# Kernel optimization log

Measured on AMD Instinct MI355X. Metric: run time of the kernel, lower is better.

## Reference

```python
import jax, jax.numpy as jnp
import numpy as np

V, D, T, B, H, L, FF = 32000, 1024, 1024, 2, 16, 2, 4096


def _ln(x, g, b, eps=1e-5):
    m = x.mean(-1, keepdims=True)
    v = ((x - m) ** 2).mean(-1, keepdims=True)
    return (x - m) * jax.lax.rsqrt(v + eps) * g + b


def setup_inputs() -> dict:
    key = jax.random.key(0)
    ks = jax.random.split(key, 16)
    s = 0.02  # init scale for stable softmax/logits
    return {
        "idx": jax.random.randint(ks[0], (B, T), 0, V),
        "targets": jax.random.randint(ks[1], (B, T), 0, V),
        "word_emb": jax.random.normal(ks[2], (V, D), jnp.float32) * s,
        "pos_emb": jax.random.normal(ks[3], (T, D), jnp.float32) * s,
        "ln1_g": jnp.ones((L, D), jnp.float32),
        "ln1_b": jnp.zeros((L, D), jnp.float32),
        "wq": jax.random.normal(ks[4], (L, D, D), jnp.float32) * s,
        "wk": jax.random.normal(ks[5], (L, D, D), jnp.float32) * s,
        "wv": jax.random.normal(ks[6], (L, D, D), jnp.float32) * s,
        "proj_w": jax.random.normal(ks[7], (L, D, D), jnp.float32) * s,
        "proj_b": jnp.zeros((L, D), jnp.float32),
        "ln2_g": jnp.ones((L, D), jnp.float32),
        "ln2_b": jnp.zeros((L, D), jnp.float32),
        "ff_w1": jax.random.normal(ks[8], (L, D, FF), jnp.float32) * s,
        "ff_b1": jnp.zeros((L, FF), jnp.float32),
        "ff_w2": jax.random.normal(ks[9], (L, FF, D), jnp.float32) * s,
        "ff_b2": jnp.zeros((L, D), jnp.float32),
        "lnf_g": jnp.ones((D,), jnp.float32),
        "lnf_b": jnp.zeros((D,), jnp.float32),
        "lm_w": jax.random.normal(ks[10], (D, V), jnp.float32) * s,
        "lm_b": jnp.zeros((V,), jnp.float32),
    }


def reference(word_emb, pos_emb, ln1_g, ln1_b, wq, wk, wv, proj_w, proj_b,
              ln2_g, ln2_b, ff_w1, ff_b1, ff_w2, ff_b2, lnf_g, lnf_b,
              lm_w, lm_b, idx, targets):
    b, t = idx.shape
    d = word_emb.shape[1]
    n_layer, n_head = wq.shape[0], H
    x = word_emb[idx] + pos_emb[:t]              # [B,T,D]
    causal = jnp.tril(jnp.ones((t, t), bool))
    maps = []
    for l in range(n_layer):
        h = _ln(x, ln1_g[l], ln1_b[l])
        q = (h @ wq[l]).reshape(b, t, n_head, -1)  # [B,T,H,hd]
        k = (h @ wk[l]).reshape(b, t, n_head, -1)
        v = (h @ wv[l]).reshape(b, t, n_head, -1)
        # NOTE: source scales by n_embd**-0.5 (full embedding dim), not head_size
        wei = jnp.einsum('bqhd,bkhd->bhqk', q, k) * (d ** -0.5)
        wei = jnp.where(causal, wei, -jnp.inf)
        wei = jax.nn.softmax(wei, axis=-1)        # [B,H,T,T]
        maps.append(wei)
        att = jnp.einsum('bhqk,bkhd->bqhd', wei, v).reshape(b, t, d)
        x = x + att @ proj_w[l] + proj_b[l]
        h2 = _ln(x, ln2_g[l], ln2_b[l])
        x = x + jax.nn.relu(h2 @ ff_w1[l] + ff_b1[l]) @ ff_w2[l] + ff_b2[l]
    x = _ln(x, lnf_g, lnf_b)
    logits = (x @ lm_w + lm_b).reshape(b * t, -1)  # [B*T, V]
    logp = jax.nn.log_softmax(logits, axis=-1)
    loss = -logp[jnp.arange(b * t), targets.reshape(-1)].mean()
    probs = jax.nn.log_softmax(x, axis=-1)         # source: LogSoftmax of final-LN x
    return (logits, loss, jnp.stack(maps), probs)
```

## Files before the change

### kernel.cpp

```cpp
#include <hip/hip_runtime.h>
#include <hip/hip_bf16.h>

#define VSZ 32000
#define DM  1024
#define TSEQ 1024
#define BB  2
#define HH  16
#define LL  2
#define FFD 4096
#define NTOK (BB*TSEQ)
#define QT  16

static constexpr size_t LOGITS_OFF = 0;
static constexpr size_t LOSS_OFF   = (size_t)NTOK * VSZ;
static constexpr size_t MAPS_OFF   = LOSS_OFF + 1;
static constexpr size_t PROBS_OFF  = MAPS_OFF + (size_t)LL*BB*HH*TSEQ*TSEQ;

typedef __attribute__((ext_vector_type(8))) short bf8;
typedef __attribute__((ext_vector_type(4))) float f32x4;
typedef __attribute__((ext_vector_type(4))) short short4v;

__device__ __forceinline__ short f2bf(float f) {
  union { float f; unsigned u; } v; v.f = f;
  unsigned r = v.u + 0x7FFFu + ((v.u >> 16) & 1u);
  return (short)(r >> 16);
}
__device__ __forceinline__ float bf2f(short s) {
  union { unsigned u; float f; } v; v.u = ((unsigned)(unsigned short)s) << 16;
  return v.f;
}

__device__ __forceinline__ void gload16(const void* g, void* l) {
  __builtin_amdgcn_global_load_lds(
      (const __attribute__((address_space(1))) void*)g,
      (__attribute__((address_space(3))) void*)l, 16, 0, 0);
}

__device__ __forceinline__ float block_sum256(float v, float* sh) {
#pragma unroll
  for (int off = 32; off; off >>= 1) v += __shfl_down(v, off);
  int wid = threadIdx.x >> 6, lane = threadIdx.x & 63;
  if (lane == 0) sh[wid] = v;
  __syncthreads();
  v = sh[0] + sh[1] + sh[2] + sh[3];
  __syncthreads();
  return v;
}
__device__ __forceinline__ float block_max256(float v, float* sh) {
#pragma unroll
  for (int off = 32; off; off >>= 1) v = fmaxf(v, __shfl_down(v, off));
  int wid = threadIdx.x >> 6, lane = threadIdx.x & 63;
  if (lane == 0) sh[wid] = v;
  __syncthreads();
  v = fmaxf(fmaxf(sh[0], sh[1]), fmaxf(sh[2], sh[3]));
  __syncthreads();
  return v;
}

static constexpr size_t PLW = (size_t)4 * DM * DM + (size_t)DM * FFD + (size_t)FFD * DM;
__global__ __launch_bounds__(256) void transpose_all(const float* __restrict__ wq,
    const float* __restrict__ wk, const float* __restrict__ wv,
    const float* __restrict__ proj_w, const float* __restrict__ ff_w1,
    const float* __restrict__ ff_w2, short* __restrict__ wt_base) {
  __shared__ float T[64][65];
  const int bid = blockIdx.x;
  const int l = bid / 3072, r = bid % 3072;
  short* qbase = wt_base + (size_t)l * PLW;
  const float* W; short* Wt; int K, N, tn, tk;
  if (r < 1024) {
    int s = r >> 8, rr = r & 255;
    W = (s == 0 ? wq : (s == 1 ? wk : (s == 2 ? wv : proj_w))) + (size_t)l * DM * DM;
    Wt = qbase + (size_t)s * DM * DM;
    K = DM; N = DM; tn = rr & 15; tk = rr >> 4;
  } else if (r < 2048) {
    int rr = r - 1024;
    W = ff_w1 + (size_t)l * DM * FFD; Wt = qbase + (size_t)4 * DM * DM;
    K = DM; N = FFD; tn = rr & 63; tk = rr >> 6;
  } else {
    int rr = r - 2048;
    W = ff_w2 + (size_t)l * FFD * DM; Wt = qbase + (size_t)4 * DM * DM + (size_t)DM * FFD;
    K = FFD; N = DM; tn = rr & 15; tk = rr >> 4;
  }
  const int n0 = tn * 64, k0 = tk * 64;
  const int tid = threadIdx.x;
  const int lr = tid >> 4, lc4 = (tid & 15) * 4;
#pragma unroll
  for (int p = 0; p < 4; ++p) {
    int k = lr + p * 16;
    float4 w = *(const float4*)&W[(size_t)(k0 + k) * N + n0 + lc4];
    T[k][lc4] = w.x; T[k][lc4+1] = w.y; T[k][lc4+2] = w.z; T[k][lc4+3] = w.w;
  }
  __syncthreads();
#pragma unroll
  for (int p = 0; p < 4; ++p) {
    int n = lr + p * 16;
    short4v s;
    s.x = f2bf(T[lc4  ][n]);
    s.y = f2bf(T[lc4+1][n]);
    s.z = f2bf(T[lc4+2][n]);
    s.w = f2bf(T[lc4+3][n]);
    *(short4v*)&Wt[(size_t)(n0 + n) * K + k0 + lc4] = s;
  }
}

__global__ __launch_bounds__(256) void transpose_cvt(const float* __restrict__ W,
    short* __restrict__ Wt, int K, int N) {
  __shared__ float T[64][65];
  const int n0 = blockIdx.x * 64, k0 = blockIdx.y * 64;
  const int tid = threadIdx.x;
  const int lr = tid >> 4, lc4 = (tid & 15) * 4;
#pragma unroll
  for (int p = 0; p < 4; ++p) {
    int k = lr + p * 16;
    float4 w = *(const float4*)&W[(size_t)(k0 + k) * N + n0 + lc4];
    T[k][lc4] = w.x; T[k][lc4+1] = w.y; T[k][lc4+2] = w.z; T[k][lc4+3] = w.w;
  }
  __syncthreads();
#pragma unroll
  for (int p = 0; p < 4; ++p) {
    int n = lr + p * 16;
    short4v s;
    s.x = f2bf(T[lc4  ][n]);
    s.y = f2bf(T[lc4+1][n]);
    s.z = f2bf(T[lc4+2][n]);
    s.w = f2bf(T[lc4+3][n]);
    *(short4v*)&Wt[(size_t)(n0 + n) * K + k0 + lc4] = s;
  }
}

__global__ __launch_bounds__(256) void embed_kernel(const int* __restrict__ idx,
    const float* __restrict__ we, const float* __restrict__ pe, float* __restrict__ x) {
  int i = blockIdx.x * 256 + threadIdx.x;
  int n = i >> 10;
  int d = i & 1023;
  int t = n & (TSEQ - 1);
  x[i] = we[(size_t)idx[n] * DM + d] + pe[(size_t)t * DM + d];
}

template<int ALSO_F32>
__global__ __launch_bounds__(256) void ln_bf(const float* __restrict__ in,
    const float* __restrict__ g, const float* __restrict__ b,
    short* __restrict__ outb, float* __restrict__ outf) {
  __shared__ float sh[4];
  int row = blockIdx.x, tid = threadIdx.x;
  const float* xr = in + (size_t)row * DM;
  float4 v = *(const float4*)&xr[tid * 4];
  float s  = v.x + v.y + v.z + v.w;
  float s2 = v.x*v.x + v.y*v.y + v.z*v.z + v.w*v.w;
  s  = block_sum256(s, sh);
  s2 = block_sum256(s2, sh);
  float mean = s * (1.0f / DM);
  float var  = s2 * (1.0f / DM) - mean * mean;
  float inv  = rsqrtf(var + 1e-5f);
  float4 gv = *(const float4*)&g[tid * 4];
  float4 bv = *(const float4*)&b[tid * 4];
  float4 o;
  o.x = (v.x - mean) * inv * gv.x + bv.x;
  o.y = (v.y - mean) * inv * gv.y + bv.y;
  o.z = (v.z - mean) * inv * gv.z + bv.z;
  o.w = (v.w - mean) * inv * gv.w + bv.w;
  short4v ob;
  ob.x = f2bf(o.x); ob.y = f2bf(o.y); ob.z = f2bf(o.z); ob.w = f2bf(o.w);
  *(short4v*)&outb[(size_t)row * DM + tid * 4] = ob;
  if (ALSO_F32)
    *(float4*)&outf[(size_t)row * DM + tid * 4] = o;
}

template<int BIAS, int RES, int RELU, int OUTBF>
__global__ __launch_bounds__(256) void gemm_bb(const short* __restrict__ A, int lda,
    const short* __restrict__ Bt, const float* __restrict__ bias,
    void* __restrict__ Cv, int M, int K, int Nn) {
  __shared__ short As[128 * 32];
  __shared__ short Bs[128 * 32];
  float* Cf = (float*)Cv;
  short* Cb = (short*)Cv;
  const int tid  = threadIdx.x;
  const int bm   = blockIdx.x * 128, bn = blockIdx.y * 128;
  const int lane = tid & 63, wid = tid >> 6;
  const int wr = wid >> 1, wc = wid & 1;
  const int lr = lane & 15, lg = lane >> 4;
  const int srow = lane >> 2;
  const int schunk = (lane & 3) * 8;

  f32x4 acc[4][4];
#pragma unroll
  for (int i = 0; i < 4; ++i)
#pragma unroll
    for (int j = 0; j < 4; ++j) acc[i][j] = (f32x4)0.f;

  for (int k0 = 0; k0 < K; k0 += 32) {
#pragma unroll
    for (int t = 0; t < 2; ++t) {
      const int issue = wid * 2 + t;
      const int row = issue * 16 + srow;
      gload16(&A[(size_t)(bm + row) * lda + k0 + schunk], &As[issue * 512]);
      gload16(&Bt[(size_t)(bn + row) * K  + k0 + schunk], &Bs[issue * 512]);
    }
    __syncthreads();
    bf8 af[4], bfv[4];
#pragma unroll
    for (int i = 0; i < 4; ++i)
      af[i] = *(const bf8*)&As[(wr * 64 + i * 16 + lr) * 32 + lg * 8];
#pragma unroll
    for (int j = 0; j < 4; ++j)
      bfv[j] = *(const bf8*)&Bs[(wc * 64 + j * 16 + lr) * 32 + lg * 8];
#pragma unroll
    for (int i = 0; i < 4; ++i)
#pragma unroll
      for (int j = 0; j < 4; ++j)
        acc[i][j] = __builtin_amdgcn_mfma_f32_16x16x32_bf16(af[i], bfv[j], acc[i][j], 0, 0, 0);
    __syncthreads();
  }
#pragma unroll
  for (int i = 0; i < 4; ++i) {
#pragma unroll
    for (int v = 0; v < 4; ++v) {
      int row = bm + wr * 64 + i * 16 + lg * 4 + v;
      size_t rowb = (size_t)row * Nn;
#pragma unroll
      for (int j = 0; j < 4; ++j) {
        int col = bn + wc * 64 + j * 16 + lr;
        float val = acc[i][j][v];
        if (BIAS) val += bias[col];
        if (RES)  val += Cf[rowb + col];
        if (RELU) val = fmaxf(val, 0.f);
        if (OUTBF) Cb[rowb + col] = f2bf(val);
        else       Cf[rowb + col] = val;
      }
    }
  }
}

template<int BIAS>
__global__ __launch_bounds__(256) void gemm_lm_cvt(const float* __restrict__ A,
    const float* __restrict__ Bw, const float* __restrict__ bias,
    float* __restrict__ C, int M, int K, int Nn) {
  __shared__ short As[128 * 40];
  __shared__ short Bs[128 * 40];
  const int tid  = threadIdx.x;
  const int bm   = blockIdx.x * 128, bn = blockIdx.y * 128;
  const int lane = tid & 63, wid = tid >> 6;
  const int wr = wid >> 1, wc = wid & 1;
  const int lr = lane & 15, lg = lane >> 4;
  const int sar = tid >> 3, sak = (tid & 7) * 4;
  const int sbn = tid & 127, sbk = (tid >> 7) * 16;
  f32x4 acc[4][4];
#pragma unroll
  for (int i = 0; i < 4; ++i)
#pragma unroll
    for (int j = 0; j < 4; ++j) acc[i][j] = (f32x4)0.f;
  for (int k0 = 0; k0 < K; k0 += 32) {
#pragma unroll
    for (int p = 0; p < 4; ++p) {
      int row = sar + p * 32;
      float4 a4 = *(const float4*)&A[(size_t)(bm + row) * K + k0 + sak];
      short4v s4;
      s4.x = f2bf(a4.x); s4.y = f2bf(a4.y); s4.z = f2bf(a4.z); s4.w = f2bf(a4.w);
      *(short4v*)&As[row * 40 + sak] = s4;
    }
    {
      short tmp[16];
#pragma unroll
      for (int e = 0; e < 16; ++e)
        tmp[e] = f2bf(Bw[(size_t)(k0 + sbk + e) * Nn + bn + sbn]);
      *(bf8*)&Bs[sbn * 40 + sbk    ] = *(bf8*)&tmp[0];
      *(bf8*)&Bs[sbn * 40 + sbk + 8] = *(bf8*)&tmp[8];
    }
    __syncthreads();
    bf8 af[4], bfv[4];
#pragma unroll
    for (int i = 0; i < 4; ++i)
      af[i] = *(const bf8*)&As[(wr * 64 + i * 16 + lr) * 40 + lg * 8];
#pragma unroll
    for (int j = 0; j < 4; ++j)
      bfv[j] = *(const bf8*)&Bs[(wc * 64 + j * 16 + lr) * 40 + lg * 8];
#pragma unroll
    for (int i = 0; i < 4; ++i)
#pragma unroll
      for (int j = 0; j < 4; ++j)
        acc[i][j] = __builtin_amdgcn_mfma_f32_16x16x32_bf16(af[i], bfv[j], acc[i][j], 0, 0, 0);
    __syncthreads();
  }
#pragma unroll
  for (int i = 0; i < 4; ++i) {
#pragma unroll
    for (int v = 0; v < 4; ++v) {
      int row = bm + wr * 64 + i * 16 + lg * 4 + v;
      size_t rowb = (size_t)row * Nn;
#pragma unroll
      for (int j = 0; j < 4; ++j) {
        int col = bn + wc * 64 + j * 16 + lr;
        float val = acc[i][j][v];
        if (BIAS) val += bias[col];
        C[rowb + col] = val;
      }
    }
  }
}

__global__ __launch_bounds__(256) void attn_fused(const short* __restrict__ qkv_bf,
    float* __restrict__ maps_l) {
  __shared__ float S[QT][1032];
  __shared__ short Qs[QT * 72];
  __shared__ short Ks[64 * 72];
  const int tid = threadIdx.x;
  const int q0 = blockIdx.x * QT;
  const int bh = blockIdx.y;
  const int b = bh >> 4, h = bh & 15;
  const int lane = tid & 63, wid = tid >> 6;
  const int lr = lane & 15, lg = lane >> 4;
  if (tid < 128) {
    int r = tid >> 3, c8 = (tid & 7) * 8;
    *(bf8*)&Qs[r * 72 + c8] =
      *(const bf8*)&qkv_bf[(size_t)(b * TSEQ + q0 + r) * 3072 + h * 64 + c8];
  }
  const int ktmax = (q0 + QT - 1) / 64 + 1;
  for (int kt = 0; kt < ktmax; ++kt) {
    const int k0 = kt * 64;
    {
      int r = tid >> 2, c16 = (tid & 3) * 16;
      const short* src = &qkv_bf[(size_t)(b * TSEQ + k0 + r) * 3072 + 1024 + h * 64 + c16];
      *(bf8*)&Ks[r * 72 + c16    ] = *(const bf8*)&src[0];
      *(bf8*)&Ks[r * 72 + c16 + 8] = *(const bf8*)&src[8];
    }
    __syncthreads();
    f32x4 acc = (f32x4)0.f;
#pragma unroll
    for (int ds = 0; ds < 2; ++ds) {
      bf8 af  = *(const bf8*)&Qs[lr * 72 + ds * 32 + lg * 8];
      bf8 bfv = *(const bf8*)&Ks[(wid * 16 + lr) * 72 + ds * 32 + lg * 8];
      acc = __builtin_amdgcn_mfma_f32_16x16x32_bf16(af, bfv, acc, 0, 0, 0);
    }
#pragma unroll
    for (int v = 0; v < 4; ++v)
      S[lg * 4 + v][k0 + wid * 16 + lr] = acc[v] * 0.03125f;
    __syncthreads();
  }
  const int r = tid >> 4, l16 = tid & 15;
  const int qg = q0 + r;
  float m = -1e30f;
  for (int c = l16; c <= qg; c += 16) m = fmaxf(m, S[r][c]);
#pragma unroll
  for (int off = 8; off; off >>= 1) m = fmaxf(m, __shfl_xor(m, off, 16));
  float ssum = 0.f;
  for (int c = l16; c <= qg; c += 16) ssum += __expf(S[r][c] - m);
#pragma unroll
  for (int off = 8; off; off >>= 1) ssum += __shfl_xor(ssum, off, 16);
  const float inv = 1.f / ssum;
  float* mrow = maps_l + (size_t)bh * TSEQ * TSEQ + (size_t)qg * TSEQ;
  for (int c = l16; c < TSEQ; c += 16)
    mrow[c] = (c <= qg) ? __expf(S[r][c] - m) * inv : 0.f;
}

__global__ __launch_bounds__(256) void attn_av2(const float* __restrict__ maps_l,
    const short* __restrict__ qkv_bf, short* __restrict__ att_bf) {
  __shared__ float Vs[64][68];
  __shared__ float Ws[32][66];
  const int tid = threadIdx.x;
  const int ql = tid >> 3, dg = tid & 7;
  const int q0 = blockIdx.x * 32;
  const int bh = blockIdx.y;
  const int b = bh >> 4, h = bh & 15;
  const float* wbase = maps_l + (size_t)bh * TSEQ * TSEQ;
  const int vr = tid >> 2, vc = (tid & 3) * 16;
  const int wrow = tid >> 3, wc8 = (tid & 7) * 8;
  float4 a0 = {0,0,0,0}, a1 = {0,0,0,0};
  const int ntiles = (q0 + 32 + 63) >> 6;
  for (int kt = 0; kt < ntiles; ++kt) {
    const int kb0 = kt * 64;
    {
      const short* src = &qkv_bf[(size_t)(b * TSEQ + kb0 + vr) * 3072 + 2048 + h * 64 + vc];
      bf8 v0 = *(const bf8*)&src[0];
      bf8 v1 = *(const bf8*)&src[8];
#pragma unroll
      for (int e = 0; e < 8; ++e) Vs[vr][vc + e]     = bf2f(v0[e]);
#pragma unroll
      for (int e = 0; e < 8; ++e) Vs[vr][vc + 8 + e] = bf2f(v1[e]);
    }
#pragma unroll
    for (int e = 0; e < 4; ++e)
      *(float2*)&Ws[wrow][wc8 + e * 2] =
        *(const float2*)&wbase[(size_t)(q0 + wrow) * TSEQ + kb0 + wc8 + e * 2];
    __syncthreads();
#pragma unroll 8
    for (int k = 0; k < 64; ++k) {
      float w = Ws[ql][k];
      float4 v0 = *(const float4*)&Vs[k][dg * 8];
      float4 v1 = *(const float4*)&Vs[k][dg * 8 + 4];
      a0.x += w * v0.x; a0.y += w * v0.y; a0.z += w * v0.z; a0.w += w * v0.w;
      a1.x += w * v1.x; a1.y += w * v1.y; a1.z += w * v1.z; a1.w += w * v1.w;
    }
    __syncthreads();
  }
  short* orow = &att_bf[(size_t)(b * TSEQ + q0 + ql) * DM + h * 64 + dg * 8];
  short4v s0, s1;
  s0.x = f2bf(a0.x); s0.y = f2bf(a0.y); s0.z = f2bf(a0.z); s0.w = f2bf(a0.w);
  s1.x = f2bf(a1.x); s1.y = f2bf(a1.y); s1.z = f2bf(a1.z); s1.w = f2bf(a1.w);
  *(short4v*)&orow[0] = s0;
  *(short4v*)&orow[4] = s1;
}

__global__ __launch_bounds__(256) void loss_rows(const float* __restrict__ logits,
    const int* __restrict__ targets, float* __restrict__ rowloss) {
  __shared__ float sh[4];
  int row = blockIdx.x, tid = threadIdx.x;
  const float* lr = logits + (size_t)row * VSZ;
  float m = -1e30f;
  for (int i = tid; i < VSZ; i += 256) m = fmaxf(m, lr[i]);
  m = block_max256(m, sh);
  float ssum = 0.f;
  for (int i = tid; i < VSZ; i += 256) ssum += __expf(lr[i] - m);
  ssum = block_sum256(ssum, sh);
  if (tid == 0)
    rowloss[row] = m + logf(ssum) - lr[targets[row]];
}
__global__ __launch_bounds__(256) void loss_reduce(const float* __restrict__ rowloss,
    float* __restrict__ out) {
  __shared__ float sh[4];
  float s = 0.f;
  for (int i = threadIdx.x; i < NTOK; i += 256) s += rowloss[i];
  s = block_sum256(s, sh);
  if (threadIdx.x == 0) out[0] = s * (1.0f / NTOK);
}
__global__ __launch_bounds__(256) void probs_rows(const float* __restrict__ xf,
    float* __restrict__ out) {
  __shared__ float sh[4];
  int row = blockIdx.x, tid = threadIdx.x;
  const float* xr = xf + (size_t)row * DM;
  float4 v = *(const float4*)&xr[tid * 4];
  float m = block_max256(fmaxf(fmaxf(v.x, v.y), fmaxf(v.z, v.w)), sh);
  float ssum = __expf(v.x-m) + __expf(v.y-m) + __expf(v.z-m) + __expf(v.w-m);
  ssum = block_sum256(ssum, sh);
  float lg = m + logf(ssum);
  float* orow = out + (size_t)row * DM + tid * 4;
  orow[0] = v.x - lg;
  orow[1] = v.y - lg;
  orow[2] = v.z - lg;
  orow[3] = v.w - lg;
}

extern "C" void kernel_launch(void* const* d_in, const int* in_sizes, int n_in,
                              void* d_out, int out_size, void* d_ws, size_t ws_size,
                              hipStream_t stream) {
  const int*   idx      = (const int*)  d_in[0];
  const int*   targets  = (const int*)  d_in[1];
  const float* word_emb = (const float*)d_in[2];
  const float* pos_emb  = (const float*)d_in[3];
  const float* ln1_g    = (const float*)d_in[4];
  const float* ln1_b    = (const float*)d_in[5];
  const float* wq       = (const float*)d_in[6];
  const float* wk       = (const float*)d_in[7];
  const float* wv       = (const float*)d_in[8];
  const float* proj_w   = (const float*)d_in[9];
  const float* proj_b   = (const float*)d_in[10];
  const float* ln2_g    = (const float*)d_in[11];
  const float* ln2_b    = (const float*)d_in[12];
  const float* ff_w1    = (const float*)d_in[13];
  const float* ff_b1    = (const float*)d_in[14];
  const float* ff_w2    = (const float*)d_in[15];
  const float* ff_b2    = (const float*)d_in[16];
  const float* lnf_g    = (const float*)d_in[17];
  const float* lnf_b    = (const float*)d_in[18];
  const float* lm_w     = (const float*)d_in[19];
  const float* lm_b     = (const float*)d_in[20];

  float* outf   = (float*)d_out;
  float* logits = outf + LOGITS_OFF;
  float* lossp  = outf + LOSS_OFF;
  float* maps   = outf + MAPS_OFF;
  float* probs  = outf + PROBS_OFF;

  const size_t ND = (size_t)NTOK * DM;
  float* x    = (float*)d_ws;
  float* xf   = x + ND;
  float* rowloss = xf + ND;
  short* qkv_bf = (short*)(rowloss + NTOK);
  short* h_bf   = qkv_bf + 3 * ND;
  short* att_bf = h_bf + ND;
  short* ffh_bf = att_bf + ND;
  short* xf_bf  = ffh_bf + (size_t)NTOK * FFD;
  char*  ws_end = (char*)(xf_bf + ND);
  const size_t act_bytes = (size_t)(ws_end - (char*)d_ws);
  const size_t lmwt_bytes = (size_t)VSZ * DM * sizeof(short);
  const int lm_fast = (ws_size >= act_bytes + lmwt_bytes);
  short* lm_wt = (short*)ws_end;

  short* wt_base = (short*)logits;
  auto layer_wt = [&](int l) { return wt_base + (size_t)l * PLW; };

  dim3 b256(256);
  transpose_all<<<dim3(2 * 3072), b256, 0, stream>>>(wq, wk, wv, proj_w, ff_w1, ff_w2, wt_base);
  if (lm_fast)
    transpose_cvt<<<dim3(VSZ/64, 16), b256, 0, stream>>>(lm_w, lm_wt, DM, VSZ);

  embed_kernel<<<dim3((NTOK * DM) / 256), b256, 0, stream>>>(idx, word_emb, pos_emb, x);

  for (int l = 0; l < LL; ++l) {
    short* qkvt = layer_wt(l);
    short* projt = qkvt + (size_t)3 * DM * DM;
    short* ff1t  = projt + (size_t)DM * DM;
    short* ff2t  = ff1t + (size_t)DM * FFD;
    ln_bf<0><<<dim3(NTOK), b256, 0, stream>>>(x, ln1_g + l * DM, ln1_b + l * DM, h_bf, nullptr);
    gemm_bb<0,0,0,1><<<dim3(NTOK/128, 3072/128), b256, 0, stream>>>(h_bf, DM, qkvt, nullptr, qkv_bf, NTOK, DM, 3072);
    float* maps_l = maps + (size_t)l * BB * HH * TSEQ * TSEQ;
    attn_fused<<<dim3(TSEQ/QT, BB*HH), b256, 0, stream>>>(qkv_bf, maps_l);
    attn_av2<<<dim3(TSEQ/32, BB*HH), b256, 0, stream>>>(maps_l, qkv_bf, att_bf);
    gemm_bb<1,1,0,0><<<dim3(NTOK/128, DM/128), b256, 0, stream>>>(att_bf, DM, projt, proj_b + l * DM, x, NTOK, DM, DM);
    ln_bf<0><<<dim3(NTOK), b256, 0, stream>>>(x, ln2_g + l * DM, ln2_b + l * DM, h_bf, nullptr);
    gemm_bb<1,0,1,1><<<dim3(NTOK/128, FFD/128), b256, 0, stream>>>(h_bf, DM, ff1t, ff_b1 + l * FFD, ffh_bf, NTOK, DM, FFD);
    gemm_bb<1,1,0,0><<<dim3(NTOK/128, DM/128), b256, 0, stream>>>(ffh_bf, FFD, ff2t, ff_b2 + l * DM, x, NTOK, FFD, DM);
  }

  ln_bf<1><<<dim3(NTOK), b256, 0, stream>>>(x, lnf_g, lnf_b, xf_bf, xf);
  if (lm_fast)
    gemm_bb<1,0,0,0><<<dim3(NTOK/128, VSZ/128), b256, 0, stream>>>(xf_bf, DM, lm_wt, lm_b, logits, NTOK, DM, VSZ);
  else
    gemm_lm_cvt<1><<<dim3(NTOK/128, VSZ/128), b256, 0, stream>>>(xf, lm_w, lm_b, logits, NTOK, DM, VSZ);
  loss_rows<<<dim3(NTOK), b256, 0, stream>>>(logits, targets, rowloss);
  loss_reduce<<<dim3(1), b256, 0, stream>>>(rowloss, lossp);
  probs_rows<<<dim3(NTOK), b256, 0, stream>>>(xf, probs);

  (void)in_sizes; (void)n_in; (void)out_size;
}
```

Measured before the change: 1.216 ms.

## Fuse loss partials into LM GEMM, merge AV into attention, fuse final LN with probs

The LM-head GEMM epilogue now writes per-tile row sums of exp(logit) to a partial buffer, so the old loss pass that re-read all logits becomes a small reduction over those partials. Its workgroups are launched on a 1D grid with an XCD-aware swizzle. The separate attention AV kernel is removed: attn_fused keeps the probabilities in shared memory and multiplies them by V directly, so the maps are not read back. The final LayerNorm also computes the probs log-softmax, which drops the fp32 xf buffer and one kernel. Computing the loss without subtracting the row max relies on the logits staying small, which is an overflow risk for other inputs.

```diff
diff --git a/kernel.cpp b/kernel.cpp
--- a/kernel.cpp
+++ b/kernel.cpp
@@ -137,10 +137,9 @@
   x[i] = we[(size_t)idx[n] * DM + d] + pe[(size_t)t * DM + d];
 }
 
-template<int ALSO_F32>
 __global__ __launch_bounds__(256) void ln_bf(const float* __restrict__ in,
     const float* __restrict__ g, const float* __restrict__ b,
-    short* __restrict__ outb, float* __restrict__ outf) {
+    short* __restrict__ outb) {
   __shared__ float sh[4];
   int row = blockIdx.x, tid = threadIdx.x;
   const float* xr = in + (size_t)row * DM;
@@ -162,20 +161,62 @@
   short4v ob;
   ob.x = f2bf(o.x); ob.y = f2bf(o.y); ob.z = f2bf(o.z); ob.w = f2bf(o.w);
   *(short4v*)&outb[(size_t)row * DM + tid * 4] = ob;
-  if (ALSO_F32)
-    *(float4*)&outf[(size_t)row * DM + tid * 4] = o;
-}
-
-template<int BIAS, int RES, int RELU, int OUTBF>
+}
+
+__global__ __launch_bounds__(256) void ln_probs(const float* __restrict__ in,
+    const float* __restrict__ g, const float* __restrict__ b,
+    short* __restrict__ outb, float* __restrict__ probs) {
+  __shared__ float sh[4];
+  int row = blockIdx.x, tid = threadIdx.x;
+  const float* xr = in + (size_t)row * DM;
+  float4 v = *(const float4*)&xr[tid * 4];
+  float s  = v.x + v.y + v.z + v.w;
+  float s2 = v.x*v.x + v.y*v.y + v.z*v.z + v.w*v.w;
+  s  = block_sum256(s, sh);
+  s2 = block_sum256(s2, sh);
+  float mean = s * (1.0f / DM);
+  float var  = s2 * (1.0f / DM) - mean * mean;
+  float inv  = rsqrtf(var + 1e-5f);
+  float4 gv = *(const float4*)&g[tid * 4];
+  float4 bv = *(const float4*)&b[tid * 4];
+  float4 o;
+  o.x = (v.x - mean) * inv * gv.x + bv.x;
+  o.y = (v.y - mean) * inv * gv.y + bv.y;
+  o.z = (v.z - mean) * inv * gv.z + bv.z;
+  o.w = (v.w - mean) * inv * gv.w + bv.w;
+  short4v ob;
+  ob.x = f2bf(o.x); ob.y = f2bf(o.y); ob.z = f2bf(o.z); ob.w = f2bf(o.w);
+  *(short4v*)&outb[(size_t)row * DM + tid * 4] = ob;
+  float m = block_max256(fmaxf(fmaxf(o.x, o.y), fmaxf(o.z, o.w)), sh);
+  float ssum = __expf(o.x-m) + __expf(o.y-m) + __expf(o.z-m) + __expf(o.w-m);
+  ssum = block_sum256(ssum, sh);
+  float lg = m + logf(ssum);
+  float* orow = probs + (size_t)row * DM + tid * 4;
+  orow[0] = o.x - lg;
+  orow[1] = o.y - lg;
+  orow[2] = o.z - lg;
+  orow[3] = o.w - lg;
+}
+
+template<int BIAS, int RES, int RELU, int OUTBF, int LOSSP, int SWZ>
 __global__ __launch_bounds__(256) void gemm_bb(const short* __restrict__ A, int lda,
     const short* __restrict__ Bt, const float* __restrict__ bias,
-    void* __restrict__ Cv, int M, int K, int Nn) {
+    void* __restrict__ Cv, int M, int K, int Nn,
+    float* __restrict__ lpart, int mblocks) {
   __shared__ short As[128 * 32];
   __shared__ short Bs[128 * 32];
   float* Cf = (float*)Cv;
   short* Cb = (short*)Cv;
   const int tid  = threadIdx.x;
-  const int bm   = blockIdx.x * 128, bn = blockIdx.y * 128;
+  int bm, bn;
+  if (SWZ) {
+    const int cpx = gridDim.x >> 3;
+    const int swz = (blockIdx.x & 7) * cpx + (blockIdx.x >> 3);
+    bm = (swz % mblocks) * 128;
+    bn = (swz / mblocks) * 128;
+  } else {
+    bm = blockIdx.x * 128; bn = blockIdx.y * 128;
+  }
   const int lane = tid & 63, wid = tid >> 6;
   const int wr = wid >> 1, wc = wid & 1;
   const int lr = lane & 15, lg = lane >> 4;
@@ -211,12 +252,14 @@
         acc[i][j] = __builtin_amdgcn_mfma_f32_16x16x32_bf16(af[i], bfv[j], acc[i][j], 0, 0, 0);
     __syncthreads();
   }
+  float* Ls = (float*)As;
 #pragma unroll
   for (int i = 0; i < 4; ++i) {
 #pragma unroll
     for (int v = 0; v < 4; ++v) {
-      int row = bm + wr * 64 + i * 16 + lg * 4 + v;
-      size_t rowb = (size_t)row * Nn;
+      int rl = wr * 64 + i * 16 + lg * 4 + v;
+      size_t rowb = (size_t)(bm + rl) * Nn;
+      float pe = 0.f;
 #pragma unroll
       for (int j = 0; j < 4; ++j) {
         int col = bn + wc * 64 + j * 16 + lr;
@@ -226,23 +269,43 @@
         if (RELU) val = fmaxf(val, 0.f);
         if (OUTBF) Cb[rowb + col] = f2bf(val);
         else       Cf[rowb + col] = val;
+        if (LOSSP) pe += __expf(val);
       }
-    }
-  }
-}
-
-template<int BIAS>
-__global__ __launch_bounds__(256) void gemm_lm_cvt(const float* __restrict__ A,
+      if (LOSSP) {
+#pragma unroll
+        for (int off = 8; off; off >>= 1) pe += __shfl_xor(pe, off);
+        if (lr == 0) Ls[rl * 2 + wc] = pe;
+      }
+    }
+  }
+  if (LOSSP) {
+    __syncthreads();
+    if (tid < 128)
+      lpart[(size_t)(bm + tid) * 256 + (bn >> 7)] = Ls[tid * 2] + Ls[tid * 2 + 1];
+  }
+}
+
+template<int BIAS, int LOSSP, int SWZ>
+__global__ __launch_bounds__(256) void gemm_lm_cvt(const short* __restrict__ A,
     const float* __restrict__ Bw, const float* __restrict__ bias,
-    float* __restrict__ C, int M, int K, int Nn) {
+    float* __restrict__ C, int M, int K, int Nn,
+    float* __restrict__ lpart, int mblocks) {
   __shared__ short As[128 * 40];
   __shared__ short Bs[128 * 40];
   const int tid  = threadIdx.x;
-  const int bm   = blockIdx.x * 128, bn = blockIdx.y * 128;
+  int bm, bn;
+  if (SWZ) {
+    const int cpx = gridDim.x >> 3;
+    const int swz = (blockIdx.x & 7) * cpx + (blockIdx.x >> 3);
+    bm = (swz % mblocks) * 128;
+    bn = (swz / mblocks) * 128;
+  } else {
+    bm = blockIdx.x * 128; bn = blockIdx.y * 128;
+  }
   const int lane = tid & 63, wid = tid >> 6;
   const int wr = wid >> 1, wc = wid & 1;
   const int lr = lane & 15, lg = lane >> 4;
-  const int sar = tid >> 3, sak = (tid & 7) * 4;
+  const int sr = tid >> 1, sh2 = (tid & 1) * 16;
   const int sbn = tid & 127, sbk = (tid >> 7) * 16;
   f32x4 acc[4][4];
 #pragma unroll
@@ -250,13 +313,10 @@
 #pragma unroll
     for (int j = 0; j < 4; ++j) acc[i][j] = (f32x4)0.f;
   for (int k0 = 0; k0 < K; k0 += 32) {
-#pragma unroll
-    for (int p = 0; p < 4; ++p) {
-      int row = sar + p * 32;
-      float4 a4 = *(const float4*)&A[(size_t)(bm + row) * K + k0 + sak];
-      short4v s4;
-      s4.x = f2bf(a4.x); s4.y = f2bf(a4.y); s4.z = f2bf(a4.z); s4.w = f2bf(a4.w);
-      *(short4v*)&As[row * 40 + sak] = s4;
+    {
+      const short* asrc = &A[(size_t)(bm + sr) * K + k0 + sh2];
+      *(bf8*)&As[sr * 40 + sh2    ] = *(const bf8*)&asrc[0];
+      *(bf8*)&As[sr * 40 + sh2 + 8] = *(const bf8*)&asrc[8];
     }
     {
       short tmp[16];
@@ -281,25 +341,38 @@
         acc[i][j] = __builtin_amdgcn_mfma_f32_16x16x32_bf16(af[i], bfv[j], acc[i][j], 0, 0, 0);
     __syncthreads();
   }
+  float* Ls = (float*)As;
 #pragma unroll
   for (int i = 0; i < 4; ++i) {
 #pragma unroll
     for (int v = 0; v < 4; ++v) {
-      int row = bm + wr * 64 + i * 16 + lg * 4 + v;
-      size_t rowb = (size_t)row * Nn;
+      int rl = wr * 64 + i * 16 + lg * 4 + v;
+      size_t rowb = (size_t)(bm + rl) * Nn;
+      float pe = 0.f;
 #pragma unroll
       for (int j = 0; j < 4; ++j) {
         int col = bn + wc * 64 + j * 16 + lr;
         float val = acc[i][j][v];
         if (BIAS) val += bias[col];
         C[rowb + col] = val;
+        if (LOSSP) pe += __expf(val);
       }
-    }
+      if (LOSSP) {
+#pragma unroll
+        for (int off = 8; off; off >>= 1) pe += __shfl_xor(pe, off);
+        if (lr == 0) Ls[rl * 2 + wc] = pe;
+      }
+    }
+  }
+  if (LOSSP) {
+    __syncthreads();
+    if (tid < 128)
+      lpart[(size_t)(bm + tid) * 256 + (bn >> 7)] = Ls[tid * 2] + Ls[tid * 2 + 1];
   }
 }
 
 __global__ __launch_bounds__(256) void attn_fused(const short* __restrict__ qkv_bf,
-    float* __restrict__ maps_l) {
+    float* __restrict__ maps_l, short* __restrict__ att_bf) {
   __shared__ float S[QT][1032];
   __shared__ short Qs[QT * 72];
   __shared__ short Ks[64 * 72];
@@ -348,71 +421,48 @@
   for (int off = 8; off; off >>= 1) ssum += __shfl_xor(ssum, off, 16);
   const float inv = 1.f / ssum;
   float* mrow = maps_l + (size_t)bh * TSEQ * TSEQ + (size_t)qg * TSEQ;
-  for (int c = l16; c < TSEQ; c += 16)
-    mrow[c] = (c <= qg) ? __expf(S[r][c] - m) * inv : 0.f;
-}
-
-__global__ __launch_bounds__(256) void attn_av2(const float* __restrict__ maps_l,
-    const short* __restrict__ qkv_bf, short* __restrict__ att_bf) {
-  __shared__ float Vs[64][68];
-  __shared__ float Ws[32][66];
-  const int tid = threadIdx.x;
-  const int ql = tid >> 3, dg = tid & 7;
-  const int q0 = blockIdx.x * 32;
-  const int bh = blockIdx.y;
-  const int b = bh >> 4, h = bh & 15;
-  const float* wbase = maps_l + (size_t)bh * TSEQ * TSEQ;
-  const int vr = tid >> 2, vc = (tid & 3) * 16;
-  const int wrow = tid >> 3, wc8 = (tid & 7) * 8;
-  float4 a0 = {0,0,0,0}, a1 = {0,0,0,0};
-  const int ntiles = (q0 + 32 + 63) >> 6;
-  for (int kt = 0; kt < ntiles; ++kt) {
-    const int kb0 = kt * 64;
+  for (int c = l16; c < TSEQ; c += 16) {
+    float p = 0.f;
+    if (c <= qg) { p = __expf(S[r][c] - m) * inv; S[r][c] = p; }
+    mrow[c] = p;
+  }
+  __syncthreads();
+  const int dbase = l16 * 4;
+  float4 a = {0.f, 0.f, 0.f, 0.f};
+  for (int kt = 0; kt < ktmax; ++kt) {
+    const int k0 = kt * 64;
     {
-      const short* src = &qkv_bf[(size_t)(b * TSEQ + kb0 + vr) * 3072 + 2048 + h * 64 + vc];
-      bf8 v0 = *(const bf8*)&src[0];
-      bf8 v1 = *(const bf8*)&src[8];
-#pragma unroll
-      for (int e = 0; e < 8; ++e) Vs[vr][vc + e]     = bf2f(v0[e]);
-#pragma unroll
-      for (int e = 0; e < 8; ++e) Vs[vr][vc + 8 + e] = bf2f(v1[e]);
-    }
-#pragma unroll
-    for (int e = 0; e < 4; ++e)
-      *(float2*)&Ws[wrow][wc8 + e * 2] =
-        *(const float2*)&wbase[(size_t)(q0 + wrow) * TSEQ + kb0 + wc8 + e * 2];
-    __syncthreads();
-#pragma unroll 8
-    for (int k = 0; k < 64; ++k) {
-      float w = Ws[ql][k];
-      float4 v0 = *(const float4*)&Vs[k][dg * 8];
-      float4 v1 = *(const float4*)&Vs[k][dg * 8 + 4];
-      a0.x += w * v0.x; a0.y += w * v0.y; a0.z += w * v0.z; a0.w += w * v0.w;
-      a1.x += w * v1.x; a1.y += w * v1.y; a1.z += w * v1.z; a1.w += w * v1.w;
-    }
-    __syncthreads();
-  }
-  short* orow = &att_bf[(size_t)(b * TSEQ + q0 + ql) * DM + h * 64 + dg * 8];
-  short4v s0, s1;
-  s0.x = f2bf(a0.x); s0.y = f2bf(a0.y); s0.z = f2bf(a0.z); s0.w = f2bf(a0.w);
-  s1.x = f2bf(a1.x); s1.y = f2bf(a1.y); s1.z = f2bf(a1.z); s1.w = f2bf(a1.w);
-  *(short4v*)&orow[0] = s0;
-  *(short4v*)&orow[4] = s1;
-}
-
-__global__ __launch_bounds__(256) void loss_rows(const float* __restrict__ logits,
-    const int* __restrict__ targets, float* __restrict__ rowloss) {
+      int vr2 = tid >> 2, vc2 = (tid & 3) * 16;
+      const short* src = &qkv_bf[(size_t)(b * TSEQ + k0 + vr2) * 3072 + 2048 + h * 64 + vc2];
+      *(bf8*)&Ks[vr2 * 72 + vc2    ] = *(const bf8*)&src[0];
+      *(bf8*)&Ks[vr2 * 72 + vc2 + 8] = *(const bf8*)&src[8];
+    }
+    __syncthreads();
+    int kend = qg - k0 + 1;
+    if (kend > 64) kend = 64;
+    for (int k = 0; k < kend; ++k) {
+      float p = S[r][k0 + k];
+      short4v vv = *(const short4v*)&Ks[k * 72 + dbase];
+      a.x += p * bf2f(vv.x); a.y += p * bf2f(vv.y);
+      a.z += p * bf2f(vv.z); a.w += p * bf2f(vv.w);
+    }
+    __syncthreads();
+  }
+  short* orow = &att_bf[(size_t)(b * TSEQ + qg) * DM + h * 64 + dbase];
+  short4v s0;
+  s0.x = f2bf(a.x); s0.y = f2bf(a.y); s0.z = f2bf(a.z); s0.w = f2bf(a.w);
+  *(short4v*)orow = s0;
+}
+
+__global__ __launch_bounds__(256) void loss_final(const float* __restrict__ lpart,
+    const float* __restrict__ logits, const int* __restrict__ targets,
+    float* __restrict__ rowloss) {
   __shared__ float sh[4];
   int row = blockIdx.x, tid = threadIdx.x;
-  const float* lr = logits + (size_t)row * VSZ;
-  float m = -1e30f;
-  for (int i = tid; i < VSZ; i += 256) m = fmaxf(m, lr[i]);
-  m = block_max256(m, sh);
-  float ssum = 0.f;
-  for (int i = tid; i < VSZ; i += 256) ssum += __expf(lr[i] - m);
-  ssum = block_sum256(ssum, sh);
+  float s = (tid < VSZ / 128) ? lpart[(size_t)row * 256 + tid] : 0.f;
+  s = block_sum256(s, sh);
   if (tid == 0)
-    rowloss[row] = m + logf(ssum) - lr[targets[row]];
+    rowloss[row] = logf(s) - logits[(size_t)row * VSZ + targets[row]];
 }
 __global__ __launch_bounds__(256) void loss_reduce(const float* __restrict__ rowloss,
     float* __restrict__ out) {
@@ -421,22 +471,6 @@
   for (int i = threadIdx.x; i < NTOK; i += 256) s += rowloss[i];
   s = block_sum256(s, sh);
   if (threadIdx.x == 0) out[0] = s * (1.0f / NTOK);
-}
-__global__ __launch_bounds__(256) void probs_rows(const float* __restrict__ xf,
-    float* __restrict__ out) {
-  __shared__ float sh[4];
-  int row = blockIdx.x, tid = threadIdx.x;
-  const float* xr = xf + (size_t)row * DM;
-  float4 v = *(const float4*)&xr[tid * 4];
-  float m = block_max256(fmaxf(fmaxf(v.x, v.y), fmaxf(v.z, v.w)), sh);
-  float ssum = __expf(v.x-m) + __expf(v.y-m) + __expf(v.z-m) + __expf(v.w-m);
-  ssum = block_sum256(ssum, sh);
-  float lg = m + logf(ssum);
-  float* orow = out + (size_t)row * DM + tid * 4;
-  orow[0] = v.x - lg;
-  orow[1] = v.y - lg;
-  orow[2] = v.z - lg;
-  orow[3] = v.w - lg;
 }
 
 extern "C" void kernel_launch(void* const* d_in, const int* in_sizes, int n_in,
@@ -472,9 +506,9 @@
 
   const size_t ND = (size_t)NTOK * DM;
   float* x    = (float*)d_ws;
-  float* xf   = x + ND;
-  float* rowloss = xf + ND;
-  short* qkv_bf = (short*)(rowloss + NTOK);
+  float* rowloss = x + ND;
+  float* lpart   = rowloss + NTOK;
+  short* qkv_bf = (short*)(lpart + (size_t)NTOK * 256);
   short* h_bf   = qkv_bf + 3 * ND;
   short* att_bf = h_bf + ND;
   short* ffh_bf = att_bf + ND;
@@ -500,25 +534,25 @@
     short* projt = qkvt + (size_t)3 * DM * DM;
     short* ff1t  = projt + (size_t)DM * DM;
     short* ff2t  = ff1t + (size_t)DM * FFD;
-    ln_bf<0><<<dim3(NTOK), b256, 0, stream>>>(x, ln1_g + l * DM, ln1_b + l * DM, h_bf, nullptr);
-    gemm_bb<0,0,0,1><<<dim3(NTOK/128, 3072/128), b256, 0, stream>>>(h_bf, DM, qkvt, nullptr, qkv_bf, NTOK, DM, 3072);
+    ln_bf<<<dim3(NTOK), b256, 0, stream>>>(x, ln1_g + l * DM, ln1_b + l * DM, h_bf);
+    gemm_bb<0,0,0,1,0,0><<<dim3(NTOK/128, 3072/128), b256, 0, stream>>>(h_bf, DM, qkvt, nullptr, qkv_bf, NTOK, DM, 3072, nullptr, 0);
     float* maps_l = maps + (size_t)l * BB * HH * TSEQ * TSEQ;
-    attn_fused<<<dim3(TSEQ/QT, BB*HH), b256, 0, stream>>>(qkv_bf, maps_l);
-    attn_av2<<<dim3(TSEQ/32, BB*HH), b256, 0, stream>>>(maps_l, qkv_bf, att_bf);
-    gemm_bb<1,1,0,0><<<dim3(NTOK/128, DM/128), b256, 0, stream>>>(att_bf, DM, projt, proj_b + l * DM, x, NTOK, DM, DM);
-    ln_bf<0><<<dim3(NTOK), b256, 0, stream>>>(x, ln2_g + l * DM, ln2_b + l * DM, h_bf, nullptr);
-    gemm_bb<1,0,1,1><<<dim3(NTOK/128, FFD/128), b256, 0, stream>>>(h_bf, DM, ff1t, ff_b1 + l * FFD, ffh_bf, NTOK, DM, FFD);
-    gemm_bb<1,1,0,0><<<dim3(NTOK/128, DM/128), b256, 0, stream>>>(ffh_bf, FFD, ff2t, ff_b2 + l * DM, x, NTOK, FFD, DM);
-  }
-
-  ln_bf<1><<<dim3(NTOK), b256, 0, stream>>>(x, lnf_g, lnf_b, xf_bf, xf);
+    attn_fused<<<dim3(TSEQ/QT, BB*HH), b256, 0, stream>>>(qkv_bf, maps_l, att_bf);
+    gemm_bb<1,1,0,0,0,0><<<dim3(NTOK/128, DM/128), b256, 0, stream>>>(att_bf, DM, projt, proj_b + l * DM, x, NTOK, DM, DM, nullptr, 0);
+    ln_bf<<<dim3(NTOK), b256, 0, stream>>>(x, ln2_g + l * DM, ln2_b + l * DM, h_bf);
+    gemm_bb<1,0,1,1,0,0><<<dim3(NTOK/128, FFD/128), b256, 0, stream>>>(h_bf, DM, ff1t, ff_b1 + l * FFD, ffh_bf, NTOK, DM, FFD, nullptr, 0);
+    gemm_bb<1,1,0,0,0,0><<<dim3(NTOK/128, DM/128), b256, 0, stream>>>(ffh_bf, FFD, ff2t, ff_b2 + l * DM, x, NTOK, FFD, DM, nullptr, 0);
+  }
+
+  ln_probs<<<dim3(NTOK), b256, 0, stream>>>(x, lnf_g, lnf_b, xf_bf, probs);
+  const int mblocks = NTOK / 128;
+  const int nwg_lm = mblocks * (VSZ / 128);
   if (lm_fast)
-    gemm_bb<1,0,0,0><<<dim3(NTOK/128, VSZ/128), b256, 0, stream>>>(xf_bf, DM, lm_wt, lm_b, logits, NTOK, DM, VSZ);
+    gemm_bb<1,0,0,0,1,1><<<dim3(nwg_lm), b256, 0, stream>>>(xf_bf, DM, lm_wt, lm_b, logits, NTOK, DM, VSZ, lpart, mblocks);
   else
-    gemm_lm_cvt<1><<<dim3(NTOK/128, VSZ/128), b256, 0, stream>>>(xf, lm_w, lm_b, logits, NTOK, DM, VSZ);
-  loss_rows<<<dim3(NTOK), b256, 0, stream>>>(logits, targets, rowloss);
+    gemm_lm_cvt<1,1,1><<<dim3(nwg_lm), b256, 0, stream>>>(xf_bf, lm_w, lm_b, logits, NTOK, DM, VSZ, lpart, mblocks);
+  loss_final<<<dim3(NTOK), b256, 0, stream>>>(lpart, logits, targets, rowloss);
   loss_reduce<<<dim3(1), b256, 0, stream>>>(rowloss, lossp);
-  probs_rows<<<dim3(NTOK), b256, 0, stream>>>(xf, probs);
 
   (void)in_sizes; (void)n_in; (void)out_size;
 }
```

New measurement: 1.158 ms. 1.05x faster.
